# Kernel tuning notes

Measured on AMD Instinct MI355X. Metric: run time of the kernel, lower is better.

## Reference

```python
import jax, jax.numpy as jnp
import numpy as np
from jax import lax

B, D, K = 8192, 768, 1000
M = 30
ENT_THR = 0.6
CAP = B + 1  # slot 0 = class prototype (normalized head weight row), up to B appended samples
EPS = 1e-12


def _l2norm(x):
    # matches F.normalize(p=2, dim=-1, eps=1e-12)
    n = jnp.sqrt(jnp.sum(x * x, axis=-1, keepdims=True))
    return x / jnp.maximum(n, EPS)


def setup_inputs() -> dict:
    key = jax.random.key(0)
    kz, kw, kb = jax.random.split(key, 3)
    z = jax.random.normal(kz, (B, D), dtype=jnp.float32)
    W = jax.random.normal(kw, (K, D), dtype=jnp.float32) / np.sqrt(D)
    b = jax.random.normal(kb, (K,), dtype=jnp.float32) * 0.01
    return {"z": z, "W": W, "b": b}


def reference(z, W, b):
    # ---- update(): base logits, entropy, keep mask ----
    logits = z @ W.T + b                                   # (B, K)
    y_hat = jnp.argmax(logits, axis=1)                     # (B,)
    p = jnp.clip(jax.nn.softmax(logits, axis=1), 1e-12, None)
    ent = -jnp.sum(p * jnp.log(p), axis=1)                 # (B,)
    keep = ent <= ENT_THR

    zn = _l2norm(z)                                        # (B, D)
    Wn = _l2norm(W)                                        # (K, D) initial prototypes, ent = 0

    # ---- scatter kept samples into per-class buffers ----
    # slot for sample i = 1 + (# kept samples j < i with same predicted class)
    oh = (keep[:, None] & (y_hat[:, None] == jnp.arange(K)[None, :])).astype(jnp.int32)  # (B, K)
    csum = jnp.cumsum(oh, axis=0)                          # inclusive count
    slot = csum[jnp.arange(B), y_hat]                      # 1-based -> slot index (0 is prototype)
    slot = jnp.where(keep, slot, CAP)                      # out-of-range -> dropped by scatter

    ent_buf = jnp.full((K, CAP), jnp.inf, dtype=logits.dtype)
    ent_buf = ent_buf.at[:, 0].set(0.0)                    # prototype entropy = 0
    ent_buf = ent_buf.at[y_hat, slot].set(ent, mode='drop')
    id_buf = jnp.full((K, CAP), -1, dtype=jnp.int32)       # -1 => prototype row (Wn[k]); inf-ent => empty
    id_buf = id_buf.at[y_hat, slot].set(jnp.arange(B, dtype=jnp.int32), mode='drop')

    # ---- _keep_topM_low_entropy: M lowest-entropy entries per class ----
    neg_ent, idx = lax.top_k(-ent_buf, M)                  # (K, M)
    sel_ent = -neg_ent
    sel_id = jnp.take_along_axis(id_buf, idx, axis=1)      # (K, M)
    valid = jnp.isfinite(sel_ent)                          # empty slots excluded

    # ---- predict(): centroid of surviving support vectors per class ----
    z_sel = jnp.where(sel_id[..., None] >= 0,
                      zn[jnp.clip(sel_id, 0)],             # (K, M, D) gathered samples
                      Wn[:, None, :])                      # prototype rows
    cnt = jnp.sum(valid, axis=1).astype(z.dtype)           # (K,) >= 1 always (prototype)
    C = jnp.sum(z_sel * valid[..., None].astype(z.dtype), axis=1) / cnt[:, None]
    Cn = _l2norm(C)                                        # (K, D)
    return zn @ Cn.T                                       # (B, K)
```

## Files before the change

kernel.cpp:

```cpp
#include <hip/hip_runtime.h>
#include <hip/hip_bf16.h>
#include <math.h>

#define B_N 8192
#define D_N 768
#define K_N 1000
#define NPAD 1024
#define M_TOP 30
#define ENT_THR 0.6f
#define EPS_N 1e-12f

typedef unsigned short u16;
typedef __attribute__((ext_vector_type(8))) short bf16x8;
typedef __attribute__((ext_vector_type(4))) float f32x4;

__device__ __forceinline__ u16 f2bf(float x) {
    __hip_bfloat16 h = __float2bfloat16(x);
    return *(u16*)&h;
}
__device__ __forceinline__ float bf2f(u16 u) {
    __hip_bfloat16 h;
    *(u16*)&h = u;
    return __bfloat162float(h);
}

__device__ __forceinline__ void gload16(const void* g, void* l) {
    __builtin_amdgcn_global_load_lds((const __attribute__((address_space(1))) void*)g,
                                     (__attribute__((address_space(3))) void*)l, 16, 0, 0);
}

__global__ __launch_bounds__(256) void split_z_kernel(const float* __restrict__ z,
                                                      u16* __restrict__ zh,
                                                      u16* __restrict__ zl) {
    size_t i = ((size_t)blockIdx.x * 256 + threadIdx.x) * 4;
    if (i >= (size_t)B_N * D_N) return;
    float4 v = *(const float4*)(z + i);
    u16 h0 = f2bf(v.x), h1 = f2bf(v.y), h2 = f2bf(v.z), h3 = f2bf(v.w);
    u16 l0 = f2bf(v.x - bf2f(h0)), l1 = f2bf(v.y - bf2f(h1));
    u16 l2 = f2bf(v.z - bf2f(h2)), l3 = f2bf(v.w - bf2f(h3));
    ushort4 hv = make_ushort4(h0, h1, h2, h3);
    ushort4 lv = make_ushort4(l0, l1, l2, l3);
    *(ushort4*)(zh + i) = hv;
    *(ushort4*)(zl + i) = lv;
}

__global__ __launch_bounds__(256) void conv_w_kernel(const float* __restrict__ W,
                                                     u16* __restrict__ Wh) {
    size_t i = ((size_t)blockIdx.x * 256 + threadIdx.x) * 4;
    if (i >= (size_t)NPAD * D_N) return;
    int row = (int)(i / D_N);
    ushort4 hv = make_ushort4(0, 0, 0, 0);
    if (row < K_N) {
        float4 v = *(const float4*)(W + i);
        hv = make_ushort4(f2bf(v.x), f2bf(v.y), f2bf(v.z), f2bf(v.w));
    }
    *(ushort4*)(Wh + i) = hv;
}

__global__ __launch_bounds__(256) void rownorm_inv_kernel(const float* __restrict__ X,
                                                          float* __restrict__ inv, int cols) {
    int row = blockIdx.x;
    int t = threadIdx.x;
    const float4* xr = (const float4*)(X + (size_t)row * cols);
    int n4 = cols >> 2;
    float s = 0.f;
    for (int j = t; j < n4; j += 256) {
        float4 v = xr[j];
        s += v.x * v.x + v.y * v.y + v.z * v.z + v.w * v.w;
    }
    __shared__ float red[256];
    red[t] = s; __syncthreads();
    for (int st = 128; st > 0; st >>= 1) {
        if (t < st) red[t] += red[t + st];
        __syncthreads();
    }
    if (t == 0) inv[row] = 1.0f / fmaxf(sqrtf(red[0]), EPS_N);
}

template <int SPLIT>
__global__ __launch_bounds__(256) void gemm_mfma(const u16* __restrict__ Ah,
                                                 const u16* __restrict__ Al,
                                                 const u16* __restrict__ Bh,
                                                 const u16* __restrict__ Bl,
                                                 const float* __restrict__ bias,
                                                 const float* __restrict__ rowscale,
                                                 float* __restrict__ C) {
    __shared__ __align__(16) u16 sA[128 * 32];
    __shared__ __align__(16) u16 sB[128 * 32];
    __shared__ __align__(16) u16 sAl[SPLIT ? 128 * 32 : 8];
    __shared__ __align__(16) u16 sBl[SPLIT ? 128 * 32 : 8];

    int t = threadIdx.x;
    int ln = t & 63, wv = t >> 6;
    int wr = wv >> 1, wc = wv & 1;
    int m0 = blockIdx.y * 128;
    int n0 = blockIdx.x * 128;

    f32x4 acc[4][4];
#pragma unroll
    for (int i = 0; i < 4; ++i)
#pragma unroll
        for (int j = 0; j < 4; ++j) acc[i][j] = (f32x4)0.f;

    int srow = ln >> 2;
    int kc = (ln & 3) * 8;
    int kb = (ln >> 4) * 16;
    int fr_row = ln & 15;

    for (int k0 = 0; k0 < D_N; k0 += 32) {
#pragma unroll
        for (int it = 0; it < 2; ++it) {
            int c = wv + it * 4;
            int row = c * 16 + srow;
            size_t ga = (size_t)(m0 + row) * D_N + k0 + kc;
            size_t gb = (size_t)(n0 + row) * D_N + k0 + kc;
            gload16(Ah + ga, (char*)sA + c * 1024);
            gload16(Bh + gb, (char*)sB + c * 1024);
            if (SPLIT) {
                gload16(Al + ga, (char*)sAl + c * 1024);
                gload16(Bl + gb, (char*)sBl + c * 1024);
            }
        }
        __syncthreads();

        bf16x8 ah[4], bh[4], al[4], bl[4];
#pragma unroll
        for (int f = 0; f < 4; ++f) {
            int abyte = (wr * 64 + f * 16 + fr_row) * 64 + kb;
            int bbyte = (wc * 64 + f * 16 + fr_row) * 64 + kb;
            ah[f] = *(const bf16x8*)((const char*)sA + abyte);
            bh[f] = *(const bf16x8*)((const char*)sB + bbyte);
            if (SPLIT) {
                al[f] = *(const bf16x8*)((const char*)sAl + abyte);
                bl[f] = *(const bf16x8*)((const char*)sBl + bbyte);
            }
        }
#pragma unroll
        for (int fr = 0; fr < 4; ++fr)
#pragma unroll
            for (int fc = 0; fc < 4; ++fc) {
                acc[fr][fc] = __builtin_amdgcn_mfma_f32_16x16x32_bf16(ah[fr], bh[fc], acc[fr][fc], 0, 0, 0);
                if (SPLIT) {
                    acc[fr][fc] = __builtin_amdgcn_mfma_f32_16x16x32_bf16(ah[fr], bl[fc], acc[fr][fc], 0, 0, 0);
                    acc[fr][fc] = __builtin_amdgcn_mfma_f32_16x16x32_bf16(al[fr], bh[fc], acc[fr][fc], 0, 0, 0);
                }
            }
        __syncthreads();
    }

    int lr4 = (ln >> 4) * 4;
    int lc = ln & 15;
#pragma unroll
    for (int fr = 0; fr < 4; ++fr) {
#pragma unroll
        for (int fc = 0; fc < 4; ++fc) {
            int gn = n0 + wc * 64 + fc * 16 + lc;
            if (gn >= K_N) continue;
            float bv = bias ? bias[gn] : 0.f;
#pragma unroll
            for (int r = 0; r < 4; ++r) {
                int gm = m0 + wr * 64 + fr * 16 + lr4 + r;
                float v = acc[fr][fc][r] + bv;
                if (rowscale) v *= rowscale[gm];
                C[(size_t)gm * K_N + gn] = v;
            }
        }
    }
}

__global__ __launch_bounds__(256) void row_entropy_kernel(const float* __restrict__ logits,
                                                          float* __restrict__ ent,
                                                          int* __restrict__ yhat) {
    int row = blockIdx.x;
    int t = threadIdx.x;
    const float* lr = logits + (size_t)row * K_N;
    float v[4];
    float mx = -INFINITY; int am = K_N;
#pragma unroll
    for (int j = 0; j < 4; ++j) {
        int idx = j * 256 + t;
        float val = (idx < K_N) ? lr[idx] : -INFINITY;
        v[j] = val;
        if (val > mx) { mx = val; am = idx; }
    }
    __shared__ float sv[256];
    __shared__ int si[256];
    __shared__ float sw[256];
    sv[t] = mx; si[t] = am; __syncthreads();
    for (int st = 128; st > 0; st >>= 1) {
        if (t < st) {
            float v2 = sv[t + st]; int i2 = si[t + st];
            if (v2 > sv[t] || (v2 == sv[t] && i2 < si[t])) { sv[t] = v2; si[t] = i2; }
        }
        __syncthreads();
    }
    float rmx = sv[0]; int ram = si[0];
    __syncthreads();
    float s = 0.f, w = 0.f;
#pragma unroll
    for (int j = 0; j < 4; ++j) {
        int idx = j * 256 + t;
        if (idx < K_N) {
            float d = v[j] - rmx;
            float e = expf(d);
            s += e; w += d * e;
        }
    }
    sv[t] = s; sw[t] = w; __syncthreads();
    for (int st = 128; st > 0; st >>= 1) {
        if (t < st) { sv[t] += sv[t + st]; sw[t] += sw[t + st]; }
        __syncthreads();
    }
    if (t == 0) {
        float S = sv[0];
        ent[row] = logf(S) - sw[0] / S;
        yhat[row] = ram;
    }
}

__global__ __launch_bounds__(256) void compact_keep_kernel(const float* __restrict__ ent,
                                                           const int* __restrict__ yhat,
                                                           unsigned long long* __restrict__ recs,
                                                           int* __restrict__ cnt) {
    int i = blockIdx.x * 256 + threadIdx.x;
    if (i >= B_N) return;
    float e = ent[i];
    if (e <= ENT_THR) {
        int pos = atomicAdd(cnt, 1);
        unsigned long long key = ((unsigned long long)__float_as_uint(e) << 32) |
                                 ((unsigned long long)(unsigned)yhat[i] << 13) |
                                 (unsigned)i;
        recs[pos] = key;
    }
}

__global__ __launch_bounds__(64) void select_topm_kernel(const unsigned long long* __restrict__ recs,
                                                         const int* __restrict__ cnt,
                                                         int* __restrict__ sel_ids,
                                                         int* __restrict__ n_sel) {
    int k = blockIdx.x;
    int lane = threadIdx.x;
    __shared__ unsigned long long top[M_TOP - 1];
    if (lane < M_TOP - 1) top[lane] = ~0ULL;
    __syncthreads();
    int n = *cnt;
    for (int base = 0; base < n; base += 64) {
        int i = base + lane;
        unsigned long long key = ~0ULL;
        bool match = false;
        if (i < n) {
            key = recs[i];
            match = ((int)((key >> 13) & 0x3FF) == k);
        }
        unsigned long long mball = __ballot(match);
        while (mball) {
            int b = __ffsll(mball) - 1;
            unsigned long long kv = __shfl(key, b);
            if (lane == 0) {
                if (kv < top[M_TOP - 2]) {
                    int pos = M_TOP - 2;
                    while (pos > 0 && top[pos - 1] > kv) { top[pos] = top[pos - 1]; --pos; }
                    top[pos] = kv;
                }
            }
            mball &= (mball - 1);
        }
    }
    __syncthreads();
    if (lane < M_TOP - 1) {
        unsigned long long kv = top[lane];
        sel_ids[k * (M_TOP - 1) + lane] = (kv == ~0ULL) ? -1 : (int)(kv & 0x1FFF);
    }
    unsigned long long vb = __ballot(lane < M_TOP - 1 && top[lane] != ~0ULL);
    if (lane == 0) n_sel[k] = (int)__popcll(vb);
}

__global__ __launch_bounds__(256) void centroid_kernel(const float* __restrict__ W,
                                                       const float* __restrict__ winv,
                                                       const float* __restrict__ z,
                                                       const float* __restrict__ zinv,
                                                       const int* __restrict__ sel_ids,
                                                       const int* __restrict__ n_sel,
                                                       u16* __restrict__ Ch,
                                                       u16* __restrict__ Cl) {
    int k = blockIdx.x;
    int t = threadIdx.x;
    if (k >= K_N) {
#pragma unroll
        for (int j = 0; j < 3; ++j) {
            Ch[(size_t)k * D_N + j * 256 + t] = 0;
            Cl[(size_t)k * D_N + j * 256 + t] = 0;
        }
        return;
    }
    float acc[3];
    float wi = winv[k];
#pragma unroll
    for (int j = 0; j < 3; ++j) acc[j] = W[(size_t)k * D_N + j * 256 + t] * wi;
    int ns = n_sel[k];
    for (int s = 0; s < ns; ++s) {
        int id = sel_ids[k * (M_TOP - 1) + s];
        float sc = zinv[id];
#pragma unroll
        for (int j = 0; j < 3; ++j) acc[j] += z[(size_t)id * D_N + j * 256 + t] * sc;
    }
    float invc = 1.0f / (float)(1 + ns);
    float s2 = 0.f;
#pragma unroll
    for (int j = 0; j < 3; ++j) { acc[j] *= invc; s2 += acc[j] * acc[j]; }
    __shared__ float red[256];
    __shared__ float sinv;
    red[t] = s2; __syncthreads();
    for (int st = 128; st > 0; st >>= 1) {
        if (t < st) red[t] += red[t + st];
        __syncthreads();
    }
    if (t == 0) sinv = 1.0f / fmaxf(sqrtf(red[0]), EPS_N);
    __syncthreads();
    float iv = sinv;
#pragma unroll
    for (int j = 0; j < 3; ++j) {
        float v = acc[j] * iv;
        u16 h = f2bf(v);
        u16 l = f2bf(v - bf2f(h));
        Ch[(size_t)k * D_N + j * 256 + t] = h;
        Cl[(size_t)k * D_N + j * 256 + t] = l;
    }
}

extern "C" void kernel_launch(void* const* d_in, const int* in_sizes, int n_in,
                              void* d_out, int out_size, void* d_ws, size_t ws_size,
                              hipStream_t stream) {
    const float* z = (const float*)d_in[0];
    const float* W = (const float*)d_in[1];
    const float* b = (const float*)d_in[2];
    float* out = (float*)d_out;

    char* p = (char*)d_ws;
    auto alloc = [&](size_t bytes) { void* r = (void*)p; p += (bytes + 255) & ~(size_t)255; return r; };
    float* zinv = (float*)alloc(B_N * 4);
    float* winv = (float*)alloc(K_N * 4);
    unsigned long long* recs = (unsigned long long*)alloc(B_N * 8);
    int* cnt = (int*)alloc(4);
    int* n_sel = (int*)alloc(K_N * 4);
    int* sel_ids = (int*)alloc(K_N * (M_TOP - 1) * 4);
    float* ent = (float*)alloc(B_N * 4);
    int* yhat = (int*)alloc(B_N * 4);
    u16* zh = (u16*)alloc((size_t)B_N * D_N * 2);
    u16* zl = (u16*)alloc((size_t)B_N * D_N * 2);
    u16* Wh = (u16*)alloc((size_t)NPAD * D_N * 2);
    u16* Ch = (u16*)alloc((size_t)NPAD * D_N * 2);
    u16* Cl = (u16*)alloc((size_t)NPAD * D_N * 2);

    hipMemsetAsync(cnt, 0, 4, stream);

    split_z_kernel<<<(B_N * D_N / 4 + 255) / 256, 256, 0, stream>>>(z, zh, zl);
    conv_w_kernel<<<(NPAD * D_N / 4 + 255) / 256, 256, 0, stream>>>(W, Wh);
    rownorm_inv_kernel<<<B_N, 256, 0, stream>>>(z, zinv, D_N);
    rownorm_inv_kernel<<<K_N, 256, 0, stream>>>(W, winv, D_N);

    dim3 gg(NPAD / 128, B_N / 128);
    gemm_mfma<0><<<gg, 256, 0, stream>>>(zh, nullptr, Wh, nullptr, b, nullptr, out);

    row_entropy_kernel<<<B_N, 256, 0, stream>>>(out, ent, yhat);
    compact_keep_kernel<<<B_N / 256, 256, 0, stream>>>(ent, yhat, recs, cnt);
    select_topm_kernel<<<K_N, 64, 0, stream>>>(recs, cnt, sel_ids, n_sel);
    centroid_kernel<<<NPAD, 256, 0, stream>>>(W, winv, z, zinv, sel_ids, n_sel, Ch, Cl);

    gemm_mfma<1><<<gg, 256, 0, stream>>>(zh, zl, Ch, Cl, nullptr, zinv, out);
}
```

Baseline: 200.5 us.

## Fuse prep kernels, double-buffer GEMM LDS tiles, fold keep compaction into entropy

Four preprocessing kernels become two. Each computes the row inverse norm with a wave shuffle reduction and writes the bf16 hi/lo splits from the same loaded registers, so z and W are read once instead of twice. The MFMA GEMM now double-buffers its LDS tiles, issuing the next k-tile's global-to-LDS loads before computing the current one, which doubles shared memory per block. The keep-mask compaction moves into the entropy kernel, removing a launch and the ent/yhat intermediate buffers.

Result: faster. 191.2 us (-4.6%).

```diff
diff --git a/kernel.cpp b/kernel.cpp
--- a/kernel.cpp
+++ b/kernel.cpp
@@ -29,52 +29,66 @@
                                      (__attribute__((address_space(3))) void*)l, 16, 0, 0);
 }
 
-__global__ __launch_bounds__(256) void split_z_kernel(const float* __restrict__ z,
-                                                      u16* __restrict__ zh,
-                                                      u16* __restrict__ zl) {
-    size_t i = ((size_t)blockIdx.x * 256 + threadIdx.x) * 4;
-    if (i >= (size_t)B_N * D_N) return;
-    float4 v = *(const float4*)(z + i);
-    u16 h0 = f2bf(v.x), h1 = f2bf(v.y), h2 = f2bf(v.z), h3 = f2bf(v.w);
-    u16 l0 = f2bf(v.x - bf2f(h0)), l1 = f2bf(v.y - bf2f(h1));
-    u16 l2 = f2bf(v.z - bf2f(h2)), l3 = f2bf(v.w - bf2f(h3));
-    ushort4 hv = make_ushort4(h0, h1, h2, h3);
-    ushort4 lv = make_ushort4(l0, l1, l2, l3);
-    *(ushort4*)(zh + i) = hv;
-    *(ushort4*)(zl + i) = lv;
-}
-
-__global__ __launch_bounds__(256) void conv_w_kernel(const float* __restrict__ W,
-                                                     u16* __restrict__ Wh) {
-    size_t i = ((size_t)blockIdx.x * 256 + threadIdx.x) * 4;
-    if (i >= (size_t)NPAD * D_N) return;
-    int row = (int)(i / D_N);
-    ushort4 hv = make_ushort4(0, 0, 0, 0);
-    if (row < K_N) {
-        float4 v = *(const float4*)(W + i);
-        hv = make_ushort4(f2bf(v.x), f2bf(v.y), f2bf(v.z), f2bf(v.w));
-    }
-    *(ushort4*)(Wh + i) = hv;
-}
-
-__global__ __launch_bounds__(256) void rownorm_inv_kernel(const float* __restrict__ X,
-                                                          float* __restrict__ inv, int cols) {
-    int row = blockIdx.x;
-    int t = threadIdx.x;
-    const float4* xr = (const float4*)(X + (size_t)row * cols);
-    int n4 = cols >> 2;
+__global__ __launch_bounds__(256) void prep_z_kernel(const float* __restrict__ z,
+                                                     u16* __restrict__ zh,
+                                                     u16* __restrict__ zl,
+                                                     float* __restrict__ zinv) {
+    int t = threadIdx.x;
+    int lane = t & 63;
+    int row = blockIdx.x * 4 + (t >> 6);
+    const float* zr = z + (size_t)row * D_N;
+    float4 v[3];
     float s = 0.f;
-    for (int j = t; j < n4; j += 256) {
-        float4 v = xr[j];
-        s += v.x * v.x + v.y * v.y + v.z * v.z + v.w * v.w;
-    }
-    __shared__ float red[256];
-    red[t] = s; __syncthreads();
-    for (int st = 128; st > 0; st >>= 1) {
-        if (t < st) red[t] += red[t + st];
-        __syncthreads();
-    }
-    if (t == 0) inv[row] = 1.0f / fmaxf(sqrtf(red[0]), EPS_N);
+#pragma unroll
+    for (int j = 0; j < 3; ++j) {
+        v[j] = *(const float4*)(zr + j * 256 + lane * 4);
+        s += v[j].x * v[j].x + v[j].y * v[j].y + v[j].z * v[j].z + v[j].w * v[j].w;
+    }
+#pragma unroll
+    for (int off = 32; off; off >>= 1) s += __shfl_xor(s, off);
+    if (lane == 0) zinv[row] = 1.0f / fmaxf(sqrtf(s), EPS_N);
+#pragma unroll
+    for (int j = 0; j < 3; ++j) {
+        float4 w = v[j];
+        u16 h0 = f2bf(w.x), h1 = f2bf(w.y), h2 = f2bf(w.z), h3 = f2bf(w.w);
+        ushort4 hv = make_ushort4(h0, h1, h2, h3);
+        ushort4 lv = make_ushort4(f2bf(w.x - bf2f(h0)), f2bf(w.y - bf2f(h1)),
+                                  f2bf(w.z - bf2f(h2)), f2bf(w.w - bf2f(h3)));
+        size_t o = (size_t)row * D_N + j * 256 + lane * 4;
+        *(ushort4*)(zh + o) = hv;
+        *(ushort4*)(zl + o) = lv;
+    }
+}
+
+__global__ __launch_bounds__(256) void prep_w_kernel(const float* __restrict__ W,
+                                                     u16* __restrict__ Wh,
+                                                     float* __restrict__ winv) {
+    int t = threadIdx.x;
+    int lane = t & 63;
+    int row = blockIdx.x * 4 + (t >> 6);
+    if (row >= K_N) {
+#pragma unroll
+        for (int j = 0; j < 3; ++j)
+            *(ushort4*)(Wh + (size_t)row * D_N + j * 256 + lane * 4) = make_ushort4(0, 0, 0, 0);
+        return;
+    }
+    const float* wr = W + (size_t)row * D_N;
+    float4 v[3];
+    float s = 0.f;
+#pragma unroll
+    for (int j = 0; j < 3; ++j) {
+        v[j] = *(const float4*)(wr + j * 256 + lane * 4);
+        s += v[j].x * v[j].x + v[j].y * v[j].y + v[j].z * v[j].z + v[j].w * v[j].w;
+    }
+#pragma unroll
+    for (int off = 32; off; off >>= 1) s += __shfl_xor(s, off);
+    if (lane == 0) winv[row] = 1.0f / fmaxf(sqrtf(s), EPS_N);
+#pragma unroll
+    for (int j = 0; j < 3; ++j) {
+        float4 w = v[j];
+        ushort4 hv = make_ushort4(f2bf(w.x), f2bf(w.y), f2bf(w.z), f2bf(w.w));
+        *(ushort4*)(Wh + (size_t)row * D_N + j * 256 + lane * 4) = hv;
+    }
 }
 
 template <int SPLIT>
@@ -85,10 +99,10 @@
                                                  const float* __restrict__ bias,
                                                  const float* __restrict__ rowscale,
                                                  float* __restrict__ C) {
-    __shared__ __align__(16) u16 sA[128 * 32];
-    __shared__ __align__(16) u16 sB[128 * 32];
-    __shared__ __align__(16) u16 sAl[SPLIT ? 128 * 32 : 8];
-    __shared__ __align__(16) u16 sBl[SPLIT ? 128 * 32 : 8];
+    __shared__ __align__(16) u16 sA[2][128 * 32];
+    __shared__ __align__(16) u16 sB[2][128 * 32];
+    __shared__ __align__(16) u16 sAl[SPLIT ? 2 : 1][SPLIT ? 128 * 32 : 8];
+    __shared__ __align__(16) u16 sBl[SPLIT ? 2 : 1][SPLIT ? 128 * 32 : 8];
 
     int t = threadIdx.x;
     int ln = t & 63, wv = t >> 6;
@@ -107,32 +121,39 @@
     int kb = (ln >> 4) * 16;
     int fr_row = ln & 15;
 
-    for (int k0 = 0; k0 < D_N; k0 += 32) {
+    auto STAGE = [&](int p, int k0) {
 #pragma unroll
         for (int it = 0; it < 2; ++it) {
             int c = wv + it * 4;
             int row = c * 16 + srow;
             size_t ga = (size_t)(m0 + row) * D_N + k0 + kc;
             size_t gb = (size_t)(n0 + row) * D_N + k0 + kc;
-            gload16(Ah + ga, (char*)sA + c * 1024);
-            gload16(Bh + gb, (char*)sB + c * 1024);
+            gload16(Ah + ga, (char*)sA[p] + c * 1024);
+            gload16(Bh + gb, (char*)sB[p] + c * 1024);
             if (SPLIT) {
-                gload16(Al + ga, (char*)sAl + c * 1024);
-                gload16(Bl + gb, (char*)sBl + c * 1024);
-            }
-        }
-        __syncthreads();
+                gload16(Al + ga, (char*)sAl[p] + c * 1024);
+                gload16(Bl + gb, (char*)sBl[p] + c * 1024);
+            }
+        }
+    };
+
+    constexpr int NT = D_N / 32;
+    STAGE(0, 0);
+    __syncthreads();
+    int cur = 0;
+    for (int tt = 0; tt < NT; ++tt) {
+        if (tt + 1 < NT) STAGE(cur ^ 1, (tt + 1) * 32);
 
         bf16x8 ah[4], bh[4], al[4], bl[4];
 #pragma unroll
         for (int f = 0; f < 4; ++f) {
             int abyte = (wr * 64 + f * 16 + fr_row) * 64 + kb;
             int bbyte = (wc * 64 + f * 16 + fr_row) * 64 + kb;
-            ah[f] = *(const bf16x8*)((const char*)sA + abyte);
-            bh[f] = *(const bf16x8*)((const char*)sB + bbyte);
+            ah[f] = *(const bf16x8*)((const char*)sA[cur] + abyte);
+            bh[f] = *(const bf16x8*)((const char*)sB[cur] + bbyte);
             if (SPLIT) {
-                al[f] = *(const bf16x8*)((const char*)sAl + abyte);
-                bl[f] = *(const bf16x8*)((const char*)sBl + bbyte);
+                al[f] = *(const bf16x8*)((const char*)sAl[cur] + abyte);
+                bl[f] = *(const bf16x8*)((const char*)sBl[cur] + bbyte);
             }
         }
 #pragma unroll
@@ -146,6 +167,7 @@
                 }
             }
         __syncthreads();
+        cur ^= 1;
     }
 
     int lr4 = (ln >> 4) * 4;
@@ -169,8 +191,8 @@
 }
 
 __global__ __launch_bounds__(256) void row_entropy_kernel(const float* __restrict__ logits,
-                                                          float* __restrict__ ent,
-                                                          int* __restrict__ yhat) {
+                                                          unsigned long long* __restrict__ recs,
+                                                          int* __restrict__ cnt) {
     int row = blockIdx.x;
     int t = threadIdx.x;
     const float* lr = logits + (size_t)row * K_N;
@@ -213,24 +235,14 @@
     }
     if (t == 0) {
         float S = sv[0];
-        ent[row] = logf(S) - sw[0] / S;
-        yhat[row] = ram;
-    }
-}
-
-__global__ __launch_bounds__(256) void compact_keep_kernel(const float* __restrict__ ent,
-                                                           const int* __restrict__ yhat,
-                                                           unsigned long long* __restrict__ recs,
-                                                           int* __restrict__ cnt) {
-    int i = blockIdx.x * 256 + threadIdx.x;
-    if (i >= B_N) return;
-    float e = ent[i];
-    if (e <= ENT_THR) {
-        int pos = atomicAdd(cnt, 1);
-        unsigned long long key = ((unsigned long long)__float_as_uint(e) << 32) |
-                                 ((unsigned long long)(unsigned)yhat[i] << 13) |
-                                 (unsigned)i;
-        recs[pos] = key;
+        float e = logf(S) - sw[0] / S;
+        if (e <= ENT_THR) {
+            int pos = atomicAdd(cnt, 1);
+            unsigned long long key = ((unsigned long long)__float_as_uint(e) << 32) |
+                                     ((unsigned long long)(unsigned)ram << 13) |
+                                     (unsigned)row;
+            recs[pos] = key;
+        }
     }
 }
 
@@ -344,8 +356,6 @@
     int* cnt = (int*)alloc(4);
     int* n_sel = (int*)alloc(K_N * 4);
     int* sel_ids = (int*)alloc(K_N * (M_TOP - 1) * 4);
-    float* ent = (float*)alloc(B_N * 4);
-    int* yhat = (int*)alloc(B_N * 4);
     u16* zh = (u16*)alloc((size_t)B_N * D_N * 2);
     u16* zl = (u16*)alloc((size_t)B_N * D_N * 2);
     u16* Wh = (u16*)alloc((size_t)NPAD * D_N * 2);
@@ -354,16 +364,13 @@
 
     hipMemsetAsync(cnt, 0, 4, stream);
 
-    split_z_kernel<<<(B_N * D_N / 4 + 255) / 256, 256, 0, stream>>>(z, zh, zl);
-    conv_w_kernel<<<(NPAD * D_N / 4 + 255) / 256, 256, 0, stream>>>(W, Wh);
-    rownorm_inv_kernel<<<B_N, 256, 0, stream>>>(z, zinv, D_N);
-    rownorm_inv_kernel<<<K_N, 256, 0, stream>>>(W, winv, D_N);
+    prep_z_kernel<<<B_N / 4, 256, 0, stream>>>(z, zh, zl, zinv);
+    prep_w_kernel<<<NPAD / 4, 256, 0, stream>>>(W, Wh, winv);
 
     dim3 gg(NPAD / 128, B_N / 128);
     gemm_mfma<0><<<gg, 256, 0, stream>>>(zh, nullptr, Wh, nullptr, b, nullptr, out);
 
-    row_entropy_kernel<<<B_N, 256, 0, stream>>>(out, ent, yhat);
-    compact_keep_kernel<<<B_N / 256, 256, 0, stream>>>(ent, yhat, recs, cnt);
+    row_entropy_kernel<<<B_N, 256, 0, stream>>>(out, recs, cnt);
     select_topm_kernel<<<K_N, 64, 0, stream>>>(recs, cnt, sel_ids, n_sel);
     centroid_kernel<<<NPAD, 256, 0, stream>>>(W, winv, z, zinv, sel_ids, n_sel, Ch, Cl);
 
```
